# Performance work log

Measured on AMD Instinct MI355X. Metric: run time of the kernel, lower is better.

Reference implementation:

```python
import jax, jax.numpy as jnp
from jax import lax
import numpy as np

FEA = 256
NHEADS = 8
GROUPS = 32
SCALE = 1.0 / np.sqrt(FEA // NHEADS)  # 1/sqrt(qkv_dim//nheads)


def conv2d(x, w, b=None, pad=0, groups=1):
    out = lax.conv_general_dilated(
        x, w, (1, 1), [(pad, pad), (pad, pad)],
        dimension_numbers=("NCHW", "OIHW", "NCHW"),
        feature_group_count=groups)
    return out if b is None else out + b[None, :, None, None]


def group_norm(x, w, b, groups=GROUPS, eps=1e-5):
    B, C, H, W = x.shape
    xg = x.reshape(B, groups, C // groups, H, W)
    m = xg.mean(axis=(2, 3, 4), keepdims=True)
    v = xg.var(axis=(2, 3, 4), keepdims=True)
    xg = (xg - m) * lax.rsqrt(v + eps)
    return xg.reshape(B, C, H, W) * w[None, :, None, None] + b[None, :, None, None]


def l2norm(x, eps=1e-12):  # F.normalize over channel dim
    n = jnp.sqrt(jnp.sum(x * x, axis=1, keepdims=True))
    return x / jnp.maximum(n, eps)


def attn_op(q, k, v):
    b, c, xf, yf = q.shape
    sp = lambda t: t.reshape(b, NHEADS, c // NHEADS, xf * yf)
    q, k, v = sp(q), sp(k), sp(v)
    sim = jnp.einsum("bhjn,bhkn->bhjk", q, k) * SCALE  # channel attention, [b,h,c/h,c/h]
    sim = jax.nn.softmax(sim, axis=-1)
    out = jnp.einsum("bhjk,bhkn->bhjn", sim, v)
    return out.reshape(b, c, xf, yf)


def freqca(x, gn_w, gn_b, dw_w, pw_w, pw_b, ao_w, ao_b, f1_w, f2_w, f3_w, f3_b):
    H, W = x.shape[-2:]
    x = group_norm(x, gn_w, gn_b)
    qkv = conv2d(conv2d(x, dw_w, pad=1, groups=FEA), pw_w, pw_b)  # depthwise 3x3 then 1x1 -> 3*qkv_dim
    q, k, v = jnp.split(qkv, 3, axis=1)
    q, k, v = l2norm(q), l2norm(k), l2norm(v)
    qf = jnp.fft.rfft2(q, axes=(-2, -1), norm="ortho")
    kf = jnp.fft.rfft2(k, axes=(-2, -1), norm="ortho")
    vf = jnp.fft.rfft2(v, axes=(-2, -1), norm="ortho")
    amp = attn_op(jnp.abs(qf), jnp.abs(kf), jnp.abs(vf))
    phas = attn_op(jnp.angle(qf), jnp.angle(kf), jnp.angle(vf))
    out_c = amp * jnp.cos(phas) + 1j * (amp * jnp.sin(phas))  # torch.polar
    out = jnp.fft.irfft2(out_c, s=(H, W), axes=(-2, -1), norm="ortho")
    attn = conv2d(out, ao_w, ao_b) + x  # attn_res is Identity (fea_dim == dim_out)
    h = jax.nn.silu(conv2d(attn, f1_w, pad=1))
    h = conv2d(h, f2_w, pad=1)
    h = conv2d(h, f3_w, f3_b)
    return h + attn  # DropPath in eval mode = identity


def setup_inputs() -> dict:
    key = jax.random.key(0)
    ks = jax.random.split(key, 12)
    B, C, H, W = 8, FEA, 128, 128
    s = 0.02
    return {
        "x": jax.random.normal(ks[0], (B, C, H, W), jnp.float32),
        "gn_w": jnp.ones((C,), jnp.float32),
        "gn_b": jnp.zeros((C,), jnp.float32),
        "dw_w": jax.random.normal(ks[1], (C, 1, 3, 3), jnp.float32) * s,
        "pw_w": jax.random.normal(ks[2], (3 * C, C, 1, 1), jnp.float32) * s,
        "pw_b": jnp.zeros((3 * C,), jnp.float32),
        "ao_w": jax.random.normal(ks[3], (C, C, 1, 1), jnp.float32) * s,
        "ao_b": jnp.zeros((C,), jnp.float32),
        "f1_w": jax.random.normal(ks[4], (2 * C, C, 3, 3), jnp.float32) * s,
        "f2_w": jax.random.normal(ks[5], (C, 2 * C, 3, 3), jnp.float32) * s,
        "f3_w": jax.random.normal(ks[6], (C, C, 1, 1), jnp.float32) * s,
        "f3_b": jnp.zeros((C,), jnp.float32),
    }


def reference(x, gn_w, gn_b, dw_w, pw_w, pw_b, ao_w, ao_b, f1_w, f2_w, f3_w, f3_b):
    return freqca(x, gn_w, gn_b, dw_w, pw_w, pw_b, ao_w, ao_b, f1_w, f2_w, f3_w, f3_b)
```

## Files before the change

### kernel.cpp

```cpp
#include <hip/hip_runtime.h>
#include <hip/hip_bf16.h>
#include <math.h>


#define TWO_PI_D 6.283185307179586476925286766559
#define ATTN_SCALE 0.17677669529663687f

typedef __attribute__((ext_vector_type(8))) short short8;
typedef __attribute__((ext_vector_type(4))) short short4v;
typedef __attribute__((ext_vector_type(4))) float f32x4;

__device__ inline short f2bf(float f) {
    __hip_bfloat16 h = __float2bfloat16(f);
    return *reinterpret_cast<short*>(&h);
}

__global__ __launch_bounds__(256) void groupnorm_kernel(
    const float* __restrict__ x, const float* __restrict__ gw,
    const float* __restrict__ gb, float* __restrict__ out, int b0)
{
    int t = threadIdx.x;
    int lb = blockIdx.x >> 5;
    int g  = blockIdx.x & 31;
    size_t src = ((size_t)(b0 + lb) * 32 + g) * 131072;
    size_t dst = (size_t)blockIdx.x * 131072;
    const float* xp = x + src;
    double s = 0.0, ss = 0.0;
    for (int i = t; i < 131072; i += 256) { double v = xp[i]; s += v; ss += v*v; }
    __shared__ double rs[256], rss[256];
    rs[t] = s; rss[t] = ss;
    __syncthreads();
    for (int k = 128; k > 0; k >>= 1) {
        if (t < k) { rs[t] += rs[t+k]; rss[t] += rss[t+k]; }
        __syncthreads();
    }
    __shared__ float smean, sinv;
    if (t == 0) {
        double mean = rs[0] * (1.0/131072.0);
        double var  = rss[0] * (1.0/131072.0) - mean*mean;
        smean = (float)mean;
        sinv  = (float)(1.0 / sqrt(var + 1e-5));
    }
    __syncthreads();
    float mean = smean, inv = sinv;
    for (int i = t; i < 131072; i += 256) {
        int c = (g << 3) + (i >> 14);
        out[dst + i] = (xp[i] - mean) * inv * gw[c] + gb[c];
    }
}

__global__ __launch_bounds__(256) void dwconv_kernel(
    const float* __restrict__ in, const float* __restrict__ w, float* __restrict__ out)
{
    int t = threadIdx.x;
    int bc = blockIdx.x >> 6;
    int y  = ((blockIdx.x & 63) << 1) + (t >> 7);
    int x  = t & 127;
    int c  = bc & 255;
    const float* wp = w + c*9;
    const float* ip = in + ((size_t)bc << 14);
    float acc = 0.f;
    #pragma unroll
    for (int dy = 0; dy < 3; dy++) {
        int yy = y + dy - 1;
        if (yy < 0 || yy > 127) continue;
        const float* row = ip + (yy << 7);
        #pragma unroll
        for (int dx = 0; dx < 3; dx++) {
            int xx = x + dx - 1;
            if (xx >= 0 && xx <= 127) acc += wp[dy*3+dx] * row[xx];
        }
    }
    out[((size_t)bc << 14) + (y << 7) + x] = acc;
}

template<int R>
__global__ __launch_bounds__(256) void conv_kernel(
    const float* __restrict__ in, const float* __restrict__ wt,
    const float* __restrict__ bias, const float* __restrict__ res,
    float* __restrict__ out, int Cin, int Cout, int act,
    int in_b0, int res_b0, int out_b0)
{
    const int K = Cin * R * R;
    int pBase  = blockIdx.x << 7;
    int coBase = blockIdx.y << 7;
    int lb = blockIdx.z;
    int t = threadIdx.x;
    int tx = t & 15, ty = t >> 4;

    __shared__ float As[8][128];
    __shared__ float Bs[8][128];

    float acc[8][8];
    #pragma unroll
    for (int i = 0; i < 8; i++)
        #pragma unroll
        for (int j = 0; j < 8; j++) acc[i][j] = 0.f;

    int a_co = t >> 1;
    int a_k  = (t & 1) << 2;
    int b_k  = t >> 5;
    int b_p  = (t & 31) << 2;
    const float* wrow = wt + (size_t)(coBase + a_co) * K + a_k;
    const size_t inb = ((size_t)(in_b0 + lb) * Cin) << 14;

    for (int k0 = 0; k0 < K; k0 += 8) {
        float4 av = *(const float4*)(wrow + k0);
        int kk = k0 + b_k;
        float4 bv = *(const float4*)(in + inb + ((size_t)kk << 14) + pBase + b_p);
        __syncthreads();
        As[a_k+0][a_co] = av.x; As[a_k+1][a_co] = av.y;
        As[a_k+2][a_co] = av.z; As[a_k+3][a_co] = av.w;
        *(float4*)&Bs[b_k][b_p] = bv;
        __syncthreads();
        #pragma unroll
        for (int k2 = 0; k2 < 8; k2++) {
            float4 A1 = *(const float4*)&As[k2][ty << 2];
            float4 A2 = *(const float4*)&As[k2][64 + (ty << 2)];
            float4 B1 = *(const float4*)&Bs[k2][tx << 2];
            float4 B2 = *(const float4*)&Bs[k2][64 + (tx << 2)];
            float a0[8] = {A1.x,A1.y,A1.z,A1.w,A2.x,A2.y,A2.z,A2.w};
            float b0v[8] = {B1.x,B1.y,B1.z,B1.w,B2.x,B2.y,B2.z,B2.w};
            #pragma unroll
            for (int i = 0; i < 8; i++)
                #pragma unroll
                for (int j = 0; j < 8; j++) acc[i][j] += a0[i] * b0v[j];
        }
    }

    #pragma unroll
    for (int i = 0; i < 8; i++) {
        int co = coBase + ((i < 4) ? ((ty << 2) + i) : (64 + (ty << 2) + i - 4));
        size_t rbo = (((size_t)(out_b0 + lb) * Cout + co) << 14) + pBase;
        size_t rbr = (((size_t)(res_b0 + lb) * Cout + co) << 14) + pBase;
        float vb = bias ? bias[co] : 0.f;
        #pragma unroll
        for (int jh = 0; jh < 2; jh++) {
            int colo = (jh == 0) ? (tx << 2) : (64 + (tx << 2));
            float4 v;
            v.x = acc[i][jh*4+0] + vb;
            v.y = acc[i][jh*4+1] + vb;
            v.z = acc[i][jh*4+2] + vb;
            v.w = acc[i][jh*4+3] + vb;
            if (act == 1) {
                v.x = v.x / (1.f + expf(-v.x));
                v.y = v.y / (1.f + expf(-v.y));
                v.z = v.z / (1.f + expf(-v.z));
                v.w = v.w / (1.f + expf(-v.w));
            }
            if (res) {
                float4 r4 = *(const float4*)(res + rbr + colo);
                v.x += r4.x; v.y += r4.y; v.z += r4.z; v.w += r4.w;
            }
            *(float4*)(out + rbo + colo) = v;
        }
    }
}

__global__ __launch_bounds__(256) void l2inv_kernel(
    const float* __restrict__ qkv, float* __restrict__ invn)
{
    int p  = ((blockIdx.x & 63) << 8) + threadIdx.x;
    int bT = blockIdx.x >> 6;
    int lb = bT / 3, T = bT - 3*lb;
    const float* base = qkv + (((size_t)(lb*768 + T*256)) << 14) + p;
    double ss = 0.0;
    for (int c = 0; c < 256; c++) { double v = base[(size_t)c << 14]; ss += v*v; }
    invn[((size_t)bT << 14) + p] = 1.f / fmaxf((float)sqrt(ss), 1e-12f);
}

__global__ __launch_bounds__(256) void fft_row_kernel(
    const float* __restrict__ qkv, const float* __restrict__ invn,
    float* __restrict__ rre, float* __restrict__ rim, int chunkBase)
{
    int rc  = blockIdx.x;
    int loc = blockIdx.y;
    int gp  = chunkBase + loc;
    int t   = threadIdx.x;
    __shared__ float xs[16][128];
    __shared__ float ex[16][64], od[16][64];
    __shared__ float x0s[16], x64s[16];
    __shared__ float ct[128], st[128];
    if (t < 128) { double s, c; sincos(TWO_PI_D * t / 128.0, &s, &c);
                   st[t] = (float)s; ct[t] = (float)c; }
    int lb = gp / 768, chn = gp - lb*768, T = chn >> 8;
    const float4* src = (const float4*)(qkv + ((size_t)gp << 14) + ((size_t)rc << 11));
    const float4* ivp = (const float4*)(invn + (((size_t)(lb*3 + T)) << 14) + ((size_t)rc << 11));
    float4* xd = (float4*)xs;
    for (int i = t; i < 512; i += 256) {
        float4 v = src[i], w = ivp[i];
        v.x *= w.x; v.y *= w.y; v.z *= w.z; v.w *= w.w;
        xd[i] = v;
    }
    __syncthreads();
    for (int i = t; i < 1008; i += 256) {
        int r = i / 63, w = i - r*63 + 1;
        float a = xs[r][w], b = xs[r][128 - w];
        ex[r][w] = a + b;
        od[r][w] = a - b;
    }
    if (t < 16) { x0s[t] = xs[t][0]; x64s[t] = xs[t][64]; }
    __syncthreads();
    for (int oo = t; oo < 260; oo += 256) {
        int k = oo % 65, rq = oo / 65;
        int r0i = rq << 2;
        float sgn = (k & 1) ? -1.f : 1.f;
        float re0 = x0s[r0i+0] + sgn*x64s[r0i+0];
        float re1 = x0s[r0i+1] + sgn*x64s[r0i+1];
        float re2 = x0s[r0i+2] + sgn*x64s[r0i+2];
        float re3 = x0s[r0i+3] + sgn*x64s[r0i+3];
        float im0 = 0.f, im1 = 0.f, im2 = 0.f, im3 = 0.f;
        int m = k;
        for (int w = 1; w < 64; w++) {
            float cc = ct[m], sn = st[m];
            re0 += ex[r0i+0][w]*cc; im0 -= od[r0i+0][w]*sn;
            re1 += ex[r0i+1][w]*cc; im1 -= od[r0i+1][w]*sn;
            re2 += ex[r0i+2][w]*cc; im2 -= od[r0i+2][w]*sn;
            re3 += ex[r0i+3][w]*cc; im3 -= od[r0i+3][w]*sn;
            m = (m + k) & 127;
        }
        size_t base = ((size_t)loc*128 + rc*16 + (rq << 2))*65 + k;
        rre[base]       = re0*0.0078125f; rim[base]       = im0*0.0078125f;
        rre[base + 65]  = re1*0.0078125f; rim[base + 65]  = im1*0.0078125f;
        rre[base + 130] = re2*0.0078125f; rim[base + 130] = im2*0.0078125f;
        rre[base + 195] = re3*0.0078125f; rim[base + 195] = im3*0.0078125f;
    }
}

__global__ __launch_bounds__(256) void fft_col_kernel(
    const float* __restrict__ rre, const float* __restrict__ rim,
    float* __restrict__ spec, int chunkBase, size_t slotStride)
{
    int kb  = blockIdx.x * 13;
    int loc = blockIdx.y;
    int gp  = chunkBase + loc;
    int t   = threadIdx.x;
    __shared__ float zr[128][14], zi[128][14];
    __shared__ float gr[8][16][14], gi[8][16][14];
    __shared__ float ct[128], st[128];
    if (t < 128) { double s, c; sincos(TWO_PI_D * t / 128.0, &s, &c);
                   st[t] = (float)s; ct[t] = (float)c; }
    for (int i = t; i < 1664; i += 256) {
        int r = i / 13, k = i - r*13;
        size_t si = ((size_t)loc*128 + r)*65 + kb + k;
        zr[r][k] = rre[si];
        zi[r][k] = rim[si];
    }
    __syncthreads();
    for (int i = t; i < 1664; i += 256) {
        int kx = i % 13, rm = i / 13;
        int r0 = rm >> 4, m = rm & 15;
        int step = (m << 3) & 127;
        float gre = 0.f, gim = 0.f;
        int idx = 0;
        for (int r1 = 0; r1 < 16; r1++) {
            float cc = ct[idx], sn = st[idx];
            float a = zr[(r1 << 3) + r0][kx], b = zi[(r1 << 3) + r0][kx];
            gre += a*cc + b*sn;
            gim += b*cc - a*sn;
            idx = (idx + step) & 127;
        }
        gr[r0][m][kx] = gre;
        gi[r0][m][kx] = gim;
    }
    __syncthreads();
    int lb = gp / 768; int chn = gp - lb*768;
    int T = chn >> 8;  int c = chn & 255;
    float* aD = spec + (size_t)(2*T)   * slotStride + ((size_t)(lb*256 + c))*8320;
    float* pD = spec + (size_t)(2*T+1) * slotStride + ((size_t)(lb*256 + c))*8320;
    for (int i = t; i < 1664; i += 256) {
        int kx = i % 13, k1 = i / 13;
        int m = k1 & 15;
        float re = 0.f, im = 0.f;
        int idx = 0;
        for (int r0 = 0; r0 < 8; r0++) {
            float cc = ct[idx], sn = st[idx];
            float a = gr[r0][m][kx], b = gi[r0][m][kx];
            re += a*cc + b*sn;
            im += b*cc - a*sn;
            idx = (idx + k1) & 127;
        }
        int kxv = kb + kx;
        if ((k1 == 0 || k1 == 64) && (kxv == 0 || kxv == 64)) im = 0.f;
        int oi = k1*65 + kxv;
        aD[oi] = sqrtf(re*re + im*im);
        pD[oi] = atan2f(im, re);
    }
}

__global__ __launch_bounds__(256) void attn_sim_kernel(
    const float* __restrict__ qA, const float* __restrict__ kA,
    float* __restrict__ simpart)
{
    int sp = blockIdx.x;
    int bh = blockIdx.y;
    int lb = bh >> 3, h = bh & 7;
    int t = threadIdx.x;
    __shared__ float qs[32][132], ks[32][132];
    const float* qb = qA + ((size_t)(lb*256 + h*32)) * 8320;
    const float* kb = kA + ((size_t)(lb*256 + h*32)) * 8320;
    float acc[4] = {0.f, 0.f, 0.f, 0.f};
    int j0 = t >> 5;
    int kq = t & 31;
    for (int sub = 0; sub < 4; sub++) {
        int n0 = sp*520 + sub*130;
        __syncthreads();
        for (int i = t; i < 4160; i += 256) {
            int j = i / 130, nn = i - j*130;
            qs[j][nn] = qb[(size_t)j*8320 + n0 + nn];
            ks[j][nn] = kb[(size_t)j*8320 + n0 + nn];
        }
        __syncthreads();
        for (int nn = 0; nn < 128; nn += 4) {
            float4 kv = *(const float4*)&ks[kq][nn];
            #pragma unroll
            for (int e = 0; e < 4; e++) {
                float4 qv = *(const float4*)&qs[j0 + e*8][nn];
                acc[e] += qv.x*kv.x + qv.y*kv.y + qv.z*kv.z + qv.w*kv.w;
            }
        }
        {
            float2 kv = *(const float2*)&ks[kq][128];
            #pragma unroll
            for (int e = 0; e < 4; e++) {
                float2 qv = *(const float2*)&qs[j0 + e*8][128];
                acc[e] += qv.x*kv.x + qv.y*kv.y;
            }
        }
    }
    float* dst = simpart + ((size_t)bh*16 + sp) * 1024;
    dst[t]       = acc[0];
    dst[t + 256] = acc[1];
    dst[t + 512] = acc[2];
    dst[t + 768] = acc[3];
}

__global__ __launch_bounds__(256) void attn_out_kernel(
    const float* __restrict__ simpart, const float* __restrict__ vA,
    float* __restrict__ outA)
{
    int nb = blockIdx.x << 8;
    int bh = blockIdx.y;
    int lb = bh >> 3, h = bh & 7;
    int t = threadIdx.x;
    __shared__ float sim[32][32];
    for (int e = t; e < 1024; e += 256) {
        float s = 0.f;
        const float* pp = simpart + (size_t)bh*16384 + e;
        #pragma unroll
        for (int sp = 0; sp < 16; sp++) s += pp[sp*1024];
        sim[e >> 5][e & 31] = s * ATTN_SCALE;
    }
    __syncthreads();
    if (t < 32) {
        float m = -1e30f;
        for (int k = 0; k < 32; k++) m = fmaxf(m, sim[t][k]);
        float s = 0.f;
        for (int k = 0; k < 32; k++) s += expf(sim[t][k] - m);
        float inv = 1.f / s;
        for (int k = 0; k < 32; k++) sim[t][k] = expf(sim[t][k] - m) * inv;
    }
    __syncthreads();
    int n = nb + t;
    if (n >= 8320) return;
    const float* vb = vA + ((size_t)(lb*256 + h*32)) * 8320 + n;
    float vv[32];
    #pragma unroll
    for (int k = 0; k < 32; k++) vv[k] = vb[(size_t)k * 8320];
    float* ob = outA + ((size_t)(lb*256 + h*32)) * 8320 + n;
    for (int j = 0; j < 32; j++) {
        float o = 0.f;
        #pragma unroll
        for (int k = 0; k < 32; k++) o += sim[j][k] * vv[k];
        ob[(size_t)j * 8320] = o;
    }
}

__global__ __launch_bounds__(256) void ifft_col_kernel(
    const float* __restrict__ ampo, const float* __restrict__ pho,
    float* __restrict__ tre, float* __restrict__ tim)
{
    int kb    = blockIdx.x * 13;
    int plane = blockIdx.y;
    int t     = threadIdx.x;
    __shared__ float zr[128][14], zi[128][14];
    __shared__ float gr[8][16][14], gi[8][16][14];
    __shared__ float ct[128], st[128];
    if (t < 128) { double s, c; sincos(TWO_PI_D * t / 128.0, &s, &c);
                   st[t] = (float)s; ct[t] = (float)c; }
    const float* ab = ampo + (size_t)plane * 8320;
    const float* pb = pho  + (size_t)plane * 8320;
    for (int i = t; i < 1664; i += 256) {
        int k1 = i / 13, k = i - k1*13;
        float a = ab[k1*65 + kb + k];
        float p = pb[k1*65 + kb + k];
        float sp, cp; sincosf(p, &sp, &cp);
        zr[k1][k] = a * cp;
        zi[k1][k] = a * sp;
    }
    __syncthreads();
    for (int i = t; i < 1664; i += 256) {
        int kx = i % 13, rm = i / 13;
        int r0 = rm >> 4, m = rm & 15;
        int step = (m << 3) & 127;
        float gre = 0.f, gim = 0.f;
        int idx = 0;
        for (int r1 = 0; r1 < 16; r1++) {
            float cc = ct[idx], sn = st[idx];
            float a = zr[(r1 << 3) + r0][kx], b = zi[(r1 << 3) + r0][kx];
            gre += a*cc - b*sn;
            gim += a*sn + b*cc;
            idx = (idx + step) & 127;
        }
        gr[r0][m][kx] = gre;
        gi[r0][m][kx] = gim;
    }
    __syncthreads();
    for (int i = t; i < 1664; i += 256) {
        int kx = i % 13, y = i / 13;
        int m = y & 15;
        float re = 0.f, im = 0.f;
        int idx = 0;
        for (int r0 = 0; r0 < 8; r0++) {
            float cc = ct[idx], sn = st[idx];
            float a = gr[r0][m][kx], b = gi[r0][m][kx];
            re += a*cc - b*sn;
            im += a*sn + b*cc;
            idx = (idx + y) & 127;
        }
        size_t oi = ((size_t)plane*128 + y)*65 + kb + kx;
        tre[oi] = re;
        tim[oi] = im;
    }
}

__global__ __launch_bounds__(256) void ifft_row_kernel(
    const float* __restrict__ tre, const float* __restrict__ tim,
    float* __restrict__ spat)
{
    int rc    = blockIdx.x;
    int plane = blockIdx.y;
    int t     = threadIdx.x;
    __shared__ float tr[16][66], ti[16][66];
    __shared__ float ct[128], st[128];
    if (t < 128) { double s, c; sincos(TWO_PI_D * t / 128.0, &s, &c);
                   st[t] = (float)s; ct[t] = (float)c; }
    for (int i = t; i < 1040; i += 256) {
        int r = i / 65, k = i - r*65;
        size_t si = ((size_t)plane*128 + rc*16 + r)*65 + k;
        float sc = (k >= 1 && k < 64) ? 2.f : 1.f;
        tr[r][k] = tre[si] * sc;
        ti[r][k] = tim[si] * sc;
    }
    __syncthreads();
    for (int oo = t; oo < 260; oo += 256) {
        int x = oo % 65, rq = oo / 65;
        int r0i = rq << 2;
        float C0 = tr[r0i+0][0], C1 = tr[r0i+1][0], C2 = tr[r0i+2][0], C3 = tr[r0i+3][0];
        float S0 = 0.f, S1 = 0.f, S2 = 0.f, S3 = 0.f;
        int m = x;
        for (int k = 1; k <= 64; k++) {
            float cc = ct[m], sn = st[m];
            C0 += tr[r0i+0][k]*cc; S0 += ti[r0i+0][k]*sn;
            C1 += tr[r0i+1][k]*cc; S1 += ti[r0i+1][k]*sn;
            C2 += tr[r0i+2][k]*cc; S2 += ti[r0i+2][k]*sn;
            C3 += tr[r0i+3][k]*cc; S3 += ti[r0i+3][k]*sn;
            m = (m + x) & 127;
        }
        size_t ob = ((size_t)plane << 14) + ((rc*16 + r0i) << 7);
        spat[ob + x]       = (C0 - S0)*0.0078125f;
        spat[ob + 128 + x] = (C1 - S1)*0.0078125f;
        spat[ob + 256 + x] = (C2 - S2)*0.0078125f;
        spat[ob + 384 + x] = (C3 - S3)*0.0078125f;
        if (x >= 1 && x <= 63) {
            int xm = 128 - x;
            spat[ob + xm]       = (C0 + S0)*0.0078125f;
            spat[ob + 128 + xm] = (C1 + S1)*0.0078125f;
            spat[ob + 256 + xm] = (C2 + S2)*0.0078125f;
            spat[ob + 384 + xm] = (C3 + S3)*0.0078125f;
        }
    }
}

__global__ __launch_bounds__(256) void wcvt_kernel(
    const float* __restrict__ w, short* __restrict__ wbf,
    int Cout, int Cin, int RR)
{
    int i = blockIdx.x * 256 + threadIdx.x;
    int total = Cout * Cin * RR;
    if (i >= total) return;
    int rr = i % RR;
    int ci = (i / RR) % Cin;
    int co = i / (RR * Cin);
    wbf[((size_t)rr * Cout + co) * Cin + ci] = f2bf(w[i]);
}

__global__ __launch_bounds__(256) void convmf2_kernel(
    const float* __restrict__ in, const short* __restrict__ wbf,
    const float* __restrict__ bias, const float* __restrict__ res,
    float* __restrict__ out, short* __restrict__ out_t,
    int Cin, int Cout, int act, int in_b0, int res_b0, int out_b0)
{
    int y      = blockIdx.x;
    int coBase = blockIdx.y << 7;
    int lb = blockIdx.z;
    int t = threadIdx.x;
    int lane = t & 63;
    int wave = t >> 6;
    int wm = (wave >> 1) << 6;
    int wn = (wave & 1) << 6;

    __shared__ short As[128][40];
    __shared__ short Bs[128][40];

    f32x4 acc[4][4];
    #pragma unroll
    for (int i = 0; i < 4; i++)
        #pragma unroll
        for (int j = 0; j < 4; j++) acc[i][j] = (f32x4){0.f, 0.f, 0.f, 0.f};

    const size_t inb = ((size_t)(in_b0 + lb) * Cin) << 14;
    int lr = lane & 15;
    int kg = (lane >> 4) << 3;

    const float* inrow = in + inb + (y << 7);
    const short* wslice = wbf + (size_t)coBase * Cin;
    for (int ci0 = 0; ci0 < Cin; ci0 += 32) {
        __syncthreads();
        #pragma unroll
        for (int u = 0; u < 2; u++) {
            int ii = t + (u << 8);
            int co = ii >> 2, cg = ii & 3;
            *(short8*)&As[co][cg << 3] =
                *(const short8*)&wslice[(size_t)co * Cin + ci0 + (cg << 3)];
        }
        for (int i = t; i < 2048; i += 256) {
            int px = i & 127, chp = i >> 7;
            int ci = ci0 + (chp << 1);
            float v0 = inrow[((size_t)ci << 14) + px];
            float v1 = inrow[((size_t)(ci + 1) << 14) + px];
            unsigned u2 = (unsigned)(unsigned short)f2bf(v0)
                        | ((unsigned)(unsigned short)f2bf(v1) << 16);
            *(unsigned*)&Bs[px][chp << 1] = u2;
        }
        __syncthreads();
        short8 af[4], bf[4];
        #pragma unroll
        for (int i = 0; i < 4; i++)
            af[i] = *(const short8*)&As[wm + i*16 + lr][kg];
        #pragma unroll
        for (int j = 0; j < 4; j++)
            bf[j] = *(const short8*)&Bs[wn + j*16 + lr][kg];
        #pragma unroll
        for (int i = 0; i < 4; i++)
            #pragma unroll
            for (int j = 0; j < 4; j++)
                acc[i][j] = __builtin_amdgcn_mfma_f32_16x16x32_bf16(
                    af[i], bf[j], acc[i][j], 0, 0, 0);
    }

    int pBase = y << 7;
    int mr = (lane >> 4) << 2;
    #pragma unroll
    for (int i = 0; i < 4; i++) {
        int co0 = coBase + wm + i*16 + mr;
        #pragma unroll
        for (int j = 0; j < 4; j++) {
            int px = pBase + wn + j*16 + lr;
            float v[4];
            #pragma unroll
            for (int r = 0; r < 4; r++) {
                float vv = acc[i][j][r] + (bias ? bias[co0 + r] : 0.f);
                if (act == 1) vv = vv / (1.f + expf(-vv));
                if (res) vv += res[(((size_t)(res_b0 + lb) * Cout + co0 + r) << 14) + px];
                v[r] = vv;
            }
            if (out) {
                #pragma unroll
                for (int r = 0; r < 4; r++)
                    out[(((size_t)(out_b0 + lb) * Cout + co0 + r) << 14) + px] = v[r];
            }
            if (out_t) {
                short4v s4 = { f2bf(v[0]), f2bf(v[1]), f2bf(v[2]), f2bf(v[3]) };
                *(short4v*)&out_t[((size_t)(lb*16384 + px)) * Cout + co0] = s4;
            }
        }
    }
}

template<int R>
__global__ __launch_bounds__(256) void convmf3_kernel(
    const short* __restrict__ in_t, const short* __restrict__ wbf,
    const float* __restrict__ bias, const float* __restrict__ res,
    float* __restrict__ out, short* __restrict__ out_t,
    int Cin, int Cout, int act, int res_b0, int out_b0)
{
    int y      = blockIdx.x;
    int coBase = blockIdx.y << 7;
    int lb = blockIdx.z;
    int t = threadIdx.x;
    int lane = t & 63;
    int wave = t >> 6;
    int wm = (wave >> 1) << 6;
    int wn = (wave & 1) << 6;
    int lr = lane & 15;
    int kg = (lane >> 4) << 3;

    f32x4 acc[4][4];
    #pragma unroll
    for (int i = 0; i < 4; i++)
        #pragma unroll
        for (int j = 0; j < 4; j++) acc[i][j] = (f32x4){0.f, 0.f, 0.f, 0.f};

    const short* inb = in_t + (((size_t)lb << 14)) * Cin;
    const short8 zero8 = {0,0,0,0,0,0,0,0};

    for (int rr = 0; rr < R*R; rr++) {
        int dy = (R == 3) ? (rr / 3) : 0;
        int dx = (R == 3) ? (rr - dy*3) : 0;
        int yy = (R == 3) ? (y + dy - 1) : y;
        if (R == 3 && (yy < 0 || yy > 127)) continue;
        const short* wsl  = wbf + ((size_t)rr * Cout + coBase) * Cin;
        const short* brow = inb + ((size_t)(yy << 7)) * Cin;
        for (int ci0 = 0; ci0 < Cin; ci0 += 32) {
            short8 af[4], bf[4];
            #pragma unroll
            for (int i = 0; i < 4; i++)
                af[i] = *(const short8*)&wsl[(size_t)(wm + i*16 + lr) * Cin + ci0 + kg];
            #pragma unroll
            for (int j = 0; j < 4; j++) {
                int pxl = wn + j*16 + lr;
                int xx = (R == 3) ? (pxl + dx - 1) : pxl;
                if (R == 3 && (xx < 0 || xx > 127)) bf[j] = zero8;
                else bf[j] = *(const short8*)&brow[(size_t)xx * Cin + ci0 + kg];
            }
            #pragma unroll
            for (int i = 0; i < 4; i++)
                #pragma unroll
                for (int j = 0; j < 4; j++)
                    acc[i][j] = __builtin_amdgcn_mfma_f32_16x16x32_bf16(
                        af[i], bf[j], acc[i][j], 0, 0, 0);
        }
    }

    int pBase = y << 7;
    int mr = (lane >> 4) << 2;
    #pragma unroll
    for (int i = 0; i < 4; i++) {
        int co0 = coBase + wm + i*16 + mr;
        #pragma unroll
        for (int j = 0; j < 4; j++) {
            int px = pBase + wn + j*16 + lr;
            float v[4];
            #pragma unroll
            for (int r = 0; r < 4; r++) {
                float vv = acc[i][j][r] + (bias ? bias[co0 + r] : 0.f);
                if (act == 1) vv = vv / (1.f + expf(-vv));
                if (res) vv += res[(((size_t)(res_b0 + lb) * Cout + co0 + r) << 14) + px];
                v[r] = vv;
            }
            if (out) {
                #pragma unroll
                for (int r = 0; r < 4; r++)
                    out[(((size_t)(out_b0 + lb) * Cout + co0 + r) << 14) + px] = v[r];
            }
            if (out_t) {
                short4v s4 = { f2bf(v[0]), f2bf(v[1]), f2bf(v[2]), f2bf(v[3]) };
                *(short4v*)&out_t[((size_t)(lb*16384 + px)) * Cout + co0] = s4;
            }
        }
    }
}

extern "C" void kernel_launch(void* const* d_in, const int* in_sizes, int n_in,
                              void* d_out, int out_size, void* d_ws, size_t ws_size,
                              hipStream_t stream) {
    (void)in_sizes; (void)n_in; (void)out_size;
    const float* x    = (const float*)d_in[0];
    const float* gn_w = (const float*)d_in[1];
    const float* gn_b = (const float*)d_in[2];
    const float* dw_w = (const float*)d_in[3];
    const float* pw_w = (const float*)d_in[4];
    const float* pw_b = (const float*)d_in[5];
    const float* ao_w = (const float*)d_in[6];
    const float* ao_b = (const float*)d_in[7];
    const float* f1_w = (const float*)d_in[8];
    const float* f2_w = (const float*)d_in[9];
    const float* f3_w = (const float*)d_in[10];
    const float* f3_b = (const float*)d_in[11];
    float* outp = (float*)d_out;

    const size_t F_QKV  = 12582912;
    const size_t F_SLOT = 2129920;
    const size_t F_SPEC = 6 * F_SLOT;
    const size_t F_XN   = 4194304;
    const size_t F_E    = 4259840;
    const size_t F_SIMP = 262144;
    const size_t F_TOT  = F_QKV + F_SPEC + F_XN + F_E + F_SIMP;
    const size_t F_WB   = 1245184;

    int NB = 0;
    for (int cand : {8, 4, 2, 1}) {
        if (((size_t)cand * F_TOT + F_WB) * 4 <= ws_size) { NB = cand; break; }
    }
    if (NB == 0) return;

    float* wsf  = (float*)d_ws;
    float* qkv  = wsf;
    short* abuf = (short*)wsf;
    short* h1t  = (short*)(wsf + (size_t)NB * 2097152);
    short* h2t  = (short*)(wsf + (size_t)NB * 6291456);
    float* spec = wsf + (size_t)NB * F_QKV;
    size_t ss   = (size_t)NB * F_SLOT;
    float* tre  = spec + 2*ss;
    float* tim  = spec + 3*ss;
    float* spat = spec + 4*ss;
    float* xn   = spec + 6*ss;
    float* ebuf = xn + (size_t)NB * F_XN;
    float* dw   = ebuf;
    float* rre  = ebuf;
    float* rim  = ebuf + (size_t)NB * 2129920;
    float* simpf = ebuf + (size_t)NB * F_E;
    float* invn  = simpf;
    float* simp  = simpf;
    short* wb    = (short*)(wsf + (size_t)NB * F_TOT);
    short* wb_ao = wb;
    short* wb_f1 = wb + 65536;
    short* wb_f2 = wb + 1245184;
    short* wb_f3 = wb + 2424832;

    wcvt_kernel<<<256,  256, 0, stream>>>(ao_w, wb_ao, 256, 256, 1);
    wcvt_kernel<<<4608, 256, 0, stream>>>(f1_w, wb_f1, 512, 256, 9);
    wcvt_kernel<<<4608, 256, 0, stream>>>(f2_w, wb_f2, 256, 512, 9);
    wcvt_kernel<<<256,  256, 0, stream>>>(f3_w, wb_f3, 256, 256, 1);

    const int passes = 8 / NB;
    for (int p = 0; p < passes; p++) {
        int b0 = p * NB;
        groupnorm_kernel<<<NB*32, 256, 0, stream>>>(x, gn_w, gn_b, xn, b0);
        dwconv_kernel<<<NB*256*64, 256, 0, stream>>>(xn, dw_w, dw);
        conv_kernel<1><<<dim3(128, 6, NB), 256, 0, stream>>>(
            dw, pw_w, pw_b, nullptr, qkv, 256, 768, 0, 0, 0, 0);
        l2inv_kernel<<<NB*3*64, 256, 0, stream>>>(qkv, invn);
        for (int chunk = 0; chunk < 3; chunk++) {
            fft_row_kernel<<<dim3(8, NB*256), 256, 0, stream>>>(
                qkv, invn, rre, rim, chunk*NB*256);
            fft_col_kernel<<<dim3(5, NB*256), 256, 0, stream>>>(
                rre, rim, spec, chunk*NB*256, ss);
        }
        attn_sim_kernel<<<dim3(16, NB*8), 256, 0, stream>>>(spec + 0*ss, spec + 2*ss, simp);
        attn_out_kernel<<<dim3(33, NB*8), 256, 0, stream>>>(simp, spec + 4*ss, spec + 0*ss);
        attn_sim_kernel<<<dim3(16, NB*8), 256, 0, stream>>>(spec + 1*ss, spec + 3*ss, simp);
        attn_out_kernel<<<dim3(33, NB*8), 256, 0, stream>>>(simp, spec + 5*ss, spec + 1*ss);
        ifft_col_kernel<<<dim3(5, NB*256), 256, 0, stream>>>(spec + 0*ss, spec + 1*ss,
                                                             tre, tim);
        ifft_row_kernel<<<dim3(8, NB*256), 256, 0, stream>>>(tre, tim, spat);
        convmf2_kernel<<<dim3(128, 2, NB), 256, 0, stream>>>(
            spat, wb_ao, ao_b, xn, outp, abuf, 256, 256, 0, 0, 0, b0);
        convmf3_kernel<3><<<dim3(128, 4, NB), 256, 0, stream>>>(
            abuf, wb_f1, nullptr, nullptr, nullptr, h1t, 256, 512, 1, 0, 0);
        convmf3_kernel<3><<<dim3(128, 2, NB), 256, 0, stream>>>(
            h1t, wb_f2, nullptr, nullptr, nullptr, h2t, 512, 256, 0, 0, 0);
        convmf3_kernel<1><<<dim3(128, 2, NB), 256, 0, stream>>>(
            h2t, wb_f3, f3_b, outp, outp, nullptr, 256, 256, 0, b0, b0);
    }
}
```

Measured before the change: 7.164 ms.

## Use split-fp16 MFMA for pointwise qkv convolution instead of FP32 SIMT GEMM

Replaces the FP32 register-tiled SIMT GEMM for the 1x1 qkv projection with an MFMA 16x16x32 f16 kernel. Weights and activations are each split into fp16 hi and lo parts, and three MFMA products are accumulated to approximate FP32 accuracy. A new pre-pass converts the weights, and activations are converted while being staged into shared memory. The aim is to move the large 768x256xP GEMM onto matrix cores, at the cost of extra conversion work, strided global loads across channels, and fp16 range limits on the split values.

```diff
diff --git a/kernel.cpp b/kernel.cpp
--- a/kernel.cpp
+++ b/kernel.cpp
@@ -9,10 +9,14 @@
 typedef __attribute__((ext_vector_type(8))) short short8;
 typedef __attribute__((ext_vector_type(4))) short short4v;
 typedef __attribute__((ext_vector_type(4))) float f32x4;
+typedef _Float16 half8v __attribute__((ext_vector_type(8)));
 
 __device__ inline short f2bf(float f) {
     __hip_bfloat16 h = __float2bfloat16(f);
     return *reinterpret_cast<short*>(&h);
+}
+__device__ inline unsigned short h_bits(_Float16 h) {
+    union { _Float16 h; unsigned short u; } c; c.h = h; return c.u;
 }
 
 __global__ __launch_bounds__(256) void groupnorm_kernel(
@@ -74,85 +78,106 @@
     out[((size_t)bc << 14) + (y << 7) + x] = acc;
 }
 
-template<int R>
-__global__ __launch_bounds__(256) void conv_kernel(
-    const float* __restrict__ in, const float* __restrict__ wt,
-    const float* __restrict__ bias, const float* __restrict__ res,
-    float* __restrict__ out, int Cin, int Cout, int act,
-    int in_b0, int res_b0, int out_b0)
-{
-    const int K = Cin * R * R;
-    int pBase  = blockIdx.x << 7;
+__global__ __launch_bounds__(256) void wcvtpw_kernel(
+    const float* __restrict__ w, _Float16* __restrict__ whi,
+    _Float16* __restrict__ wlo, int total)
+{
+    int i = blockIdx.x * 256 + threadIdx.x;
+    if (i >= total) return;
+    float v = w[i];
+    _Float16 h = (_Float16)v;
+    _Float16 l = (_Float16)(v - (float)h);
+    whi[i] = h; wlo[i] = l;
+}
+
+__global__ __launch_bounds__(256) void convpw_kernel(
+    const float* __restrict__ in, const _Float16* __restrict__ whi,
+    const _Float16* __restrict__ wlo, const float* __restrict__ bias,
+    float* __restrict__ out)
+{
+    int y      = blockIdx.x;
     int coBase = blockIdx.y << 7;
-    int lb = blockIdx.z;
+    int lb     = blockIdx.z;
     int t = threadIdx.x;
-    int tx = t & 15, ty = t >> 4;
-
-    __shared__ float As[8][128];
-    __shared__ float Bs[8][128];
-
-    float acc[8][8];
+    int lane = t & 63;
+    int wave = t >> 6;
+    int wm = (wave >> 1) << 6;
+    int wn = (wave & 1) << 6;
+    int lr = lane & 15;
+    int kg = (lane >> 4) << 3;
+
+    __shared__ _Float16 Ah[128][40], Al[128][40];
+    __shared__ _Float16 Bh[128][40], Bl[128][40];
+
+    f32x4 acc[4][4];
     #pragma unroll
-    for (int i = 0; i < 8; i++)
-        #pragma unroll
-        for (int j = 0; j < 8; j++) acc[i][j] = 0.f;
-
-    int a_co = t >> 1;
-    int a_k  = (t & 1) << 2;
-    int b_k  = t >> 5;
-    int b_p  = (t & 31) << 2;
-    const float* wrow = wt + (size_t)(coBase + a_co) * K + a_k;
-    const size_t inb = ((size_t)(in_b0 + lb) * Cin) << 14;
-
-    for (int k0 = 0; k0 < K; k0 += 8) {
-        float4 av = *(const float4*)(wrow + k0);
-        int kk = k0 + b_k;
-        float4 bv = *(const float4*)(in + inb + ((size_t)kk << 14) + pBase + b_p);
+    for (int i = 0; i < 4; i++)
+        #pragma unroll
+        for (int j = 0; j < 4; j++) acc[i][j] = (f32x4){0.f, 0.f, 0.f, 0.f};
+
+    const float* inrow = in + (((size_t)lb * 256) << 14) + (y << 7);
+    for (int ci0 = 0; ci0 < 256; ci0 += 32) {
         __syncthreads();
-        As[a_k+0][a_co] = av.x; As[a_k+1][a_co] = av.y;
-        As[a_k+2][a_co] = av.z; As[a_k+3][a_co] = av.w;
-        *(float4*)&Bs[b_k][b_p] = bv;
+        #pragma unroll
+        for (int u = 0; u < 2; u++) {
+            int ii = t + (u << 8);
+            int co = ii >> 2, cg = ii & 3;
+            *(half8v*)&Ah[co][cg << 3] =
+                *(const half8v*)&whi[(size_t)(coBase + co) * 256 + ci0 + (cg << 3)];
+            *(half8v*)&Al[co][cg << 3] =
+                *(const half8v*)&wlo[(size_t)(coBase + co) * 256 + ci0 + (cg << 3)];
+        }
+        for (int i = t; i < 2048; i += 256) {
+            int px = i & 127, chp = i >> 7;
+            int ci = ci0 + (chp << 1);
+            float v0 = inrow[((size_t)ci << 14) + px];
+            float v1 = inrow[((size_t)(ci + 1) << 14) + px];
+            _Float16 h0 = (_Float16)v0, h1 = (_Float16)v1;
+            _Float16 l0 = (_Float16)(v0 - (float)h0);
+            _Float16 l1 = (_Float16)(v1 - (float)h1);
+            unsigned uh = (unsigned)h_bits(h0) | ((unsigned)h_bits(h1) << 16);
+            unsigned ul = (unsigned)h_bits(l0) | ((unsigned)h_bits(l1) << 16);
+            *(unsigned*)&Bh[px][chp << 1] = uh;
+            *(unsigned*)&Bl[px][chp << 1] = ul;
+        }
         __syncthreads();
-        #pragma unroll
-        for (int k2 = 0; k2 < 8; k2++) {
-            float4 A1 = *(const float4*)&As[k2][ty << 2];
-            float4 A2 = *(const float4*)&As[k2][64 + (ty << 2)];
-            float4 B1 = *(const float4*)&Bs[k2][tx << 2];
-            float4 B2 = *(const float4*)&Bs[k2][64 + (tx << 2)];
-            float a0[8] = {A1.x,A1.y,A1.z,A1.w,A2.x,A2.y,A2.z,A2.w};
-            float b0v[8] = {B1.x,B1.y,B1.z,B1.w,B2.x,B2.y,B2.z,B2.w};
-            #pragma unroll
-            for (int i = 0; i < 8; i++)
-                #pragma unroll
-                for (int j = 0; j < 8; j++) acc[i][j] += a0[i] * b0v[j];
-        }
-    }
-
+        half8v ah[4], al[4], bh4[4], bl4[4];
+        #pragma unroll
+        for (int i = 0; i < 4; i++) {
+            ah[i] = *(const half8v*)&Ah[wm + i*16 + lr][kg];
+            al[i] = *(const half8v*)&Al[wm + i*16 + lr][kg];
+        }
+        #pragma unroll
+        for (int j = 0; j < 4; j++) {
+            bh4[j] = *(const half8v*)&Bh[wn + j*16 + lr][kg];
+            bl4[j] = *(const half8v*)&Bl[wn + j*16 + lr][kg];
+        }
+        #pragma unroll
+        for (int i = 0; i < 4; i++)
+            #pragma unroll
+            for (int j = 0; j < 4; j++) {
+                acc[i][j] = __builtin_amdgcn_mfma_f32_16x16x32_f16(
+                    ah[i], bh4[j], acc[i][j], 0, 0, 0);
+                acc[i][j] = __builtin_amdgcn_mfma_f32_16x16x32_f16(
+                    ah[i], bl4[j], acc[i][j], 0, 0, 0);
+                acc[i][j] = __builtin_amdgcn_mfma_f32_16x16x32_f16(
+                    al[i], bh4[j], acc[i][j], 0, 0, 0);
+            }
+    }
+
+    int pBase = y << 7;
+    int mr = (lane >> 4) << 2;
     #pragma unroll
-    for (int i = 0; i < 8; i++) {
-        int co = coBase + ((i < 4) ? ((ty << 2) + i) : (64 + (ty << 2) + i - 4));
-        size_t rbo = (((size_t)(out_b0 + lb) * Cout + co) << 14) + pBase;
-        size_t rbr = (((size_t)(res_b0 + lb) * Cout + co) << 14) + pBase;
-        float vb = bias ? bias[co] : 0.f;
-        #pragma unroll
-        for (int jh = 0; jh < 2; jh++) {
-            int colo = (jh == 0) ? (tx << 2) : (64 + (tx << 2));
-            float4 v;
-            v.x = acc[i][jh*4+0] + vb;
-            v.y = acc[i][jh*4+1] + vb;
-            v.z = acc[i][jh*4+2] + vb;
-            v.w = acc[i][jh*4+3] + vb;
-            if (act == 1) {
-                v.x = v.x / (1.f + expf(-v.x));
-                v.y = v.y / (1.f + expf(-v.y));
-                v.z = v.z / (1.f + expf(-v.z));
-                v.w = v.w / (1.f + expf(-v.w));
-            }
-            if (res) {
-                float4 r4 = *(const float4*)(res + rbr + colo);
-                v.x += r4.x; v.y += r4.y; v.z += r4.z; v.w += r4.w;
-            }
-            *(float4*)(out + rbo + colo) = v;
+    for (int i = 0; i < 4; i++) {
+        int co0 = coBase + wm + i*16 + mr;
+        #pragma unroll
+        for (int j = 0; j < 4; j++) {
+            int px = pBase + wn + j*16 + lr;
+            #pragma unroll
+            for (int r = 0; r < 4; r++) {
+                out[(((size_t)(lb*768 + co0 + r)) << 14) + px] =
+                    acc[i][j][r] + bias[co0 + r];
+            }
         }
     }
 }
@@ -697,7 +722,7 @@
     const size_t F_E    = 4259840;
     const size_t F_SIMP = 262144;
     const size_t F_TOT  = F_QKV + F_SPEC + F_XN + F_E + F_SIMP;
-    const size_t F_WB   = 1245184;
+    const size_t F_WB   = 1441792;
 
     int NB = 0;
     for (int cand : {8, 4, 2, 1}) {
@@ -728,19 +753,22 @@
     short* wb_f1 = wb + 65536;
     short* wb_f2 = wb + 1245184;
     short* wb_f3 = wb + 2424832;
+    _Float16* wb_pw_hi = (_Float16*)(wb + 2490368);
+    _Float16* wb_pw_lo = (_Float16*)(wb + 2686976);
 
     wcvt_kernel<<<256,  256, 0, stream>>>(ao_w, wb_ao, 256, 256, 1);
     wcvt_kernel<<<4608, 256, 0, stream>>>(f1_w, wb_f1, 512, 256, 9);
     wcvt_kernel<<<4608, 256, 0, stream>>>(f2_w, wb_f2, 256, 512, 9);
     wcvt_kernel<<<256,  256, 0, stream>>>(f3_w, wb_f3, 256, 256, 1);
+    wcvtpw_kernel<<<768, 256, 0, stream>>>(pw_w, wb_pw_hi, wb_pw_lo, 196608);
 
     const int passes = 8 / NB;
     for (int p = 0; p < passes; p++) {
         int b0 = p * NB;
         groupnorm_kernel<<<NB*32, 256, 0, stream>>>(x, gn_w, gn_b, xn, b0);
         dwconv_kernel<<<NB*256*64, 256, 0, stream>>>(xn, dw_w, dw);
-        conv_kernel<1><<<dim3(128, 6, NB), 256, 0, stream>>>(
-            dw, pw_w, pw_b, nullptr, qkv, 256, 768, 0, 0, 0, 0);
+        convpw_kernel<<<dim3(128, 6, NB), 256, 0, stream>>>(
+            dw, wb_pw_hi, wb_pw_lo, pw_b, qkv);
         l2inv_kernel<<<NB*3*64, 256, 0, stream>>>(qkv, invn);
         for (int chunk = 0; chunk < 3; chunk++) {
             fft_row_kernel<<<dim3(8, NB*256), 256, 0, stream>>>(
```

Measured after the change: 7.023 ms. 2.0% less time.
